# Performance work log

Measured on AMD Instinct MI355X. Metric: run time of the kernel, lower is better.

## Reference

```python
import jax, jax.numpy as jnp
import numpy as np

DECAY = 0.99
EPS = 1e-05


def setup_inputs() -> dict:
    key = jax.random.key(0)
    k1, k2, k3 = jax.random.split(key, 3)
    inp = jax.random.normal(k1, (8, 1024, 512), dtype=jnp.float32)
    embed = jax.random.normal(k2, (512, 8192), dtype=jnp.float32)
    # buffers: cluster_size starts at zeros, embed_avg is a clone of embed in torch
    cluster_size = jnp.zeros((8192,), dtype=jnp.float32)
    embed_avg = embed
    return {"input": inp, "embed": embed, "cluster_size": cluster_size, "embed_avg": embed_avg}


def reference(input, embed, cluster_size, embed_avg):
    dim, n_embed = embed.shape
    flatten = input.reshape(-1, dim)  # [N, dim]
    # squared euclidean distance via expansion: ||f||^2 - 2 f.E + ||E||^2 -> [N, n_embed]
    dist = ((flatten ** 2).sum(axis=1, keepdims=True)
            - 2.0 * flatten @ embed
            + (embed ** 2).sum(axis=0, keepdims=True))
    embed_ind_flat = jnp.argmin(dist, axis=1)  # argmax of -dist == argmin of dist
    embed_ind = embed_ind_flat.reshape(input.shape[:-1])
    # nearest-codebook lookup: F.embedding(ind, embed.T)
    quantize = jnp.take(embed.T, embed_ind, axis=0)  # [..., dim]
    # training-mode EMA statistics (one-hot scatter sums, done without a dense one-hot)
    onehot_sum = jnp.zeros((n_embed,), flatten.dtype).at[embed_ind_flat].add(1.0)
    embed_sum = jax.ops.segment_sum(flatten, embed_ind_flat, num_segments=n_embed).T  # [dim, n_embed]
    new_cluster_size = cluster_size * DECAY + (1.0 - DECAY) * onehot_sum
    new_embed_avg = embed_avg * DECAY + (1.0 - DECAY) * embed_sum
    n = new_cluster_size.sum()
    cs = (new_cluster_size + EPS) / (n + n_embed * EPS) * n
    new_embed = new_embed_avg / cs[None, :]
    # commitment loss (quantize detached) and straight-through estimator
    diff = jnp.mean((jax.lax.stop_gradient(quantize) - input) ** 2)
    quantize_st = input + jax.lax.stop_gradient(quantize - input)
    return (quantize_st, diff, embed_ind, new_embed, new_cluster_size, new_embed_avg)
```

## Files before the change

### kernel.cpp

```cpp
#include <hip/hip_runtime.h>


constexpr int N = 8192;
constexpr int K = 512;
constexpr int M = 8192;

typedef unsigned short ushortT;
typedef __attribute__((ext_vector_type(8))) short s8v;
typedef __attribute__((ext_vector_type(4))) float f4v;

__device__ __forceinline__ ushortT f2bf(float x) {
    unsigned u = __float_as_uint(x);
    unsigned r = (u + 0x7FFFu + ((u >> 16) & 1u)) >> 16;
    return (ushortT)r;
}
__device__ __forceinline__ float bf2f(ushortT h) {
    return __uint_as_float(((unsigned)h) << 16);
}

typedef const __attribute__((address_space(1))) unsigned gau;
typedef __attribute__((address_space(3))) unsigned lau;
__device__ __forceinline__ void gl16(const void* g, void* l) {
    __builtin_amdgcn_global_load_lds((gau*)g, (lau*)l, 16, 0, 0);
}

__device__ __forceinline__ unsigned packDI(float d, int col) {
    unsigned u = __float_as_uint(d);
    unsigned s = (u & 0x80000000u) ? ~u : (u | 0x80000000u);
    return (s & ~0x1FFFu) | (unsigned)col;
}
__device__ __forceinline__ float unpackD(unsigned p) {
    unsigned s = p & ~0x1FFFu;
    unsigned u = (s & 0x80000000u) ? (s & 0x7fffffffu) : ~s;
    return __uint_as_float(u);
}
__device__ __forceinline__ void top2u(unsigned& a, unsigned& b, unsigned c) {
    unsigned mn = c < a ? c : a;
    unsigned mx = c < a ? a : c;
    a = mn;
    b = mx < b ? mx : b;
}

__global__ __launch_bounds__(256) void k_prep(
    const float* __restrict__ f, const float* __restrict__ E,
    ushortT* __restrict__ Fh, ushortT* __restrict__ EhT, ushortT* __restrict__ ElT,
    float* __restrict__ pc, float* __restrict__ counts) {
    __shared__ float tile[64][65];
    int b = blockIdx.x, t = threadIdx.x;
    if (b < 2048) {
        if (b < 32) counts[b * 256 + t] = 0.f;
        size_t i8 = ((size_t)b * 256 + t) * 8;
        float4 x0 = *(const float4*)&f[i8];
        float4 x1 = *(const float4*)&f[i8 + 4];
        float xs[8] = {x0.x, x0.y, x0.z, x0.w, x1.x, x1.y, x1.z, x1.w};
        union { s8v v; ushortT u[8]; } h;
#pragma unroll
        for (int j = 0; j < 8; ++j) h.u[j] = f2bf(xs[j]);
        *(s8v*)&Fh[i8] = h.v;
    } else {
        int bb = b - 2048;
        int jb = bb & 127, kb = bb >> 7;
        int jj = t & 63, kk0 = t >> 6;
        int j0 = jb * 64, k0 = kb * 64;
#pragma unroll
        for (int it = 0; it < 16; ++it) {
            int kk = it * 4 + kk0;
            tile[kk][jj] = E[(size_t)(k0 + kk) * M + j0 + jj];
        }
        __syncthreads();
        int r = t >> 2, ks = (t & 3) * 16;
        union { s8v v[2]; ushortT u[16]; } h, lo;
        float nrm = 0.f;
#pragma unroll
        for (int i = 0; i < 16; ++i) {
            float x = tile[ks + i][r];
            nrm = fmaf(x, x, nrm);
            ushortT hh = f2bf(x);
            h.u[i] = hh;
            lo.u[i] = f2bf(x - bf2f(hh));
        }
        size_t o = (size_t)(j0 + r) * K + k0 + ks;
        *(s8v*)&EhT[o] = h.v[0];
        *(s8v*)&EhT[o + 8] = h.v[1];
        *(s8v*)&ElT[o] = lo.v[0];
        *(s8v*)&ElT[o + 8] = lo.v[1];
        nrm += __shfl_down(nrm, 2);
        nrm += __shfl_down(nrm, 1);
        if ((t & 3) == 0) pc[(size_t)kb * M + j0 + r] = nrm;
    }
}

__global__ __launch_bounds__(512) void k_score(
    const ushortT* __restrict__ Fh, const ushortT* __restrict__ Eh,
    const float* __restrict__ pc, unsigned* __restrict__ pv) {
    __shared__ alignas(16) ushortT ls[2][2][256 * 64];

    int bid = blockIdx.x;
    int xcd = bid & 7, local = bid >> 3;
    int rb = xcd * 4 + (local & 3);
    int cb = local >> 2;
    int rowBase = rb * 256, colBase = cb * 256;
    int tid = threadIdx.x;
    int w = tid >> 6, l = tid & 63;
    int wr = w >> 2, wc = w & 3;
    int l15 = l & 15, g4 = l >> 4;
    int s7 = l15 & 7;

    const ushortT* srcA = Fh + (size_t)(rowBase + w * 32) * K;
    const ushortT* srcB = Eh + (size_t)(colBase + w * 32) * K;

    f4v acc[8][4];
#pragma unroll
    for (int m = 0; m < 8; ++m)
#pragma unroll
        for (int n = 0; n < 4; ++n) acc[m][n] = (f4v){0.f, 0.f, 0.f, 0.f};

#define STAGE(p, ch)                                                  \
    do {                                                              \
        _Pragma("unroll")                                             \
        for (int i_ = 0; i_ < 4; ++i_) {                              \
            int q_ = i_ * 64 + l;                                     \
            int row_ = q_ >> 3, slot_ = q_ & 7;                       \
            int swz_ = (slot_ ^ (row_ & 7)) * 8;                      \
            size_t so_ = (size_t)row_ * K + (ch) * 64 + swz_;         \
            gl16(srcA + so_, &ls[p][0][w * 2048 + q_ * 8]);           \
            gl16(srcB + so_, &ls[p][1][w * 2048 + q_ * 8]);           \
        }                                                             \
    } while (0)

    STAGE(0, 0);
    __syncthreads();

#pragma unroll
    for (int ch = 0; ch < 8; ++ch) {
        int p = ch & 1;
        if (ch < 7) STAGE(p ^ 1, ch + 1);
#pragma unroll
        for (int kk = 0; kk < 2; ++kk) {
            s8v a[8], b[4];
#pragma unroll
            for (int m = 0; m < 8; ++m) {
                int rA = wr * 128 + m * 16 + l15;
                a[m] = *(const s8v*)&ls[p][0][rA * 64 + ((kk * 4 + g4) ^ s7) * 8];
            }
#pragma unroll
            for (int n = 0; n < 4; ++n) {
                int rB = wc * 64 + n * 16 + l15;
                b[n] = *(const s8v*)&ls[p][1][rB * 64 + ((kk * 4 + g4) ^ s7) * 8];
            }
#pragma unroll
            for (int m = 0; m < 8; ++m)
#pragma unroll
                for (int n = 0; n < 4; ++n)
                    acc[m][n] = __builtin_amdgcn_mfma_f32_16x16x32_bf16(
                        a[m], b[n], acc[m][n], 0, 0, 0);
        }
        __syncthreads();
    }
#undef STAGE

    float cj[4];
#pragma unroll
    for (int n = 0; n < 4; ++n) {
        int col = colBase + wc * 64 + n * 16 + l15;
        float s = 0.f;
#pragma unroll
        for (int kb = 0; kb < 8; ++kb) s += pc[(size_t)kb * M + col];
        cj[n] = s;
    }
    unsigned* cand = (unsigned*)ls;

#pragma unroll
    for (int m = 0; m < 8; ++m)
#pragma unroll
        for (int q = 0; q < 4; ++q) {
            unsigned p0 = packDI(fmaf(-2.f, acc[m][0][q], cj[0]), colBase + wc * 64 + l15);
            unsigned p1 = packDI(fmaf(-2.f, acc[m][1][q], cj[1]), colBase + wc * 64 + 16 + l15);
            unsigned p2 = packDI(fmaf(-2.f, acc[m][2][q], cj[2]), colBase + wc * 64 + 32 + l15);
            unsigned p3 = packDI(fmaf(-2.f, acc[m][3][q], cj[3]), colBase + wc * 64 + 48 + l15);
            unsigned a_ = p0 < p1 ? p0 : p1;
            unsigned b_ = p0 < p1 ? p1 : p0;
            top2u(a_, b_, p2);
            top2u(a_, b_, p3);
#pragma unroll
            for (int mk = 8; mk >= 2; mk >>= 1) {
                unsigned oa = __shfl_xor((int)a_, mk);
                unsigned ob = __shfl_xor((int)b_, mk);
                top2u(a_, b_, oa);
                top2u(a_, b_, ob);
            }
            if (l15 < 2) {
                int row = wr * 128 + m * 16 + g4 * 4 + q;
                int slot = wc * 4 + l15 * 2;
                cand[row * 17 + slot] = a_;
                cand[row * 17 + slot + 1] = b_;
            }
        }
    __syncthreads();
    if (tid < 256) {
        unsigned best = cand[tid * 17], second = cand[tid * 17 + 1];
#pragma unroll
        for (int i = 2; i < 16; i += 2) {
            top2u(best, second, cand[tid * 17 + i]);
            top2u(best, second, cand[tid * 17 + i + 1]);
        }
        size_t o = (size_t)(rowBase + tid) * 64 + cb * 2;
        pv[o] = best;
        pv[o + 1] = second;
    }
}

__global__ __launch_bounds__(256) void k_combine(
    const unsigned* __restrict__ pv, const float* __restrict__ f,
    const ushortT* __restrict__ EhT, const ushortT* __restrict__ ElT,
    const float* __restrict__ pc,
    int* __restrict__ indws, float* __restrict__ o_ind, float* __restrict__ counts,
    float* __restrict__ o_q, float* __restrict__ diffp) {
    __shared__ float dsum[4];
    int w = threadIdx.x >> 6, l = threadIdx.x & 63;
    int row = blockIdx.x * 4 + w;
    unsigned e = pv[(size_t)row * 64 + l];
    unsigned mn = e;
#pragma unroll
    for (int m = 1; m < 64; m <<= 1) {
        unsigned o = __shfl_xor((int)mn, m);
        mn = o < mn ? o : mn;
    }
    float thr = unpackD(mn) + 2.0f;
    float dl = unpackD(e);
    float bestd = 3.4e38f; int bestj = 0x7fffffff;
    float4 fa = *(const float4*)&f[(size_t)row * K + l * 8];
    float4 fb = *(const float4*)&f[(size_t)row * K + l * 8 + 4];
    float fx[8] = {fa.x, fa.y, fa.z, fa.w, fb.x, fb.y, fb.z, fb.w};
    s8v qh, ql;
    unsigned long long mask = __ballot(dl <= thr);
    while (mask) {
        int b = __ffsll(mask) - 1;
        mask &= mask - 1;
        int j = (int)(__shfl((int)e, b) & 0x1fff);
        s8v hv = *(const s8v*)(EhT + (size_t)j * K + l * 8);
        s8v lv = *(const s8v*)(ElT + (size_t)j * K + l * 8);
        float a = 0.f;
#pragma unroll
        for (int q = 0; q < 8; ++q)
            a = fmaf(fx[q], bf2f((ushortT)hv[q]) + bf2f((ushortT)lv[q]), a);
#pragma unroll
        for (int m = 1; m < 64; m <<= 1) a += __shfl_xor(a, m);
        float cj = 0.f;
#pragma unroll
        for (int kb = 0; kb < 8; ++kb) cj += pc[(size_t)kb * M + j];
        float d = cj - 2.f * a;
        if (d < bestd || (d == bestd && j < bestj)) {
            bestd = d; bestj = j; qh = hv; ql = lv;
        }
    }
    float os[8];
    float local = 0.f;
#pragma unroll
    for (int q = 0; q < 8; ++q) {
        float qv = bf2f((ushortT)qh[q]) + bf2f((ushortT)ql[q]);
        float d = qv - fx[q];
        os[q] = fx[q] + d;
        local = fmaf(d, d, local);
    }
    float4 o0 = {os[0], os[1], os[2], os[3]};
    float4 o1 = {os[4], os[5], os[6], os[7]};
    *(float4*)&o_q[(size_t)row * K + l * 8] = o0;
    *(float4*)&o_q[(size_t)row * K + l * 8 + 4] = o1;
#pragma unroll
    for (int m = 1; m < 64; m <<= 1) local += __shfl_xor(local, m);
    if (l == 0) {
        indws[row] = bestj;
        o_ind[row] = (float)bestj;
        atomicAdd(&counts[bestj], 1.0f);
        dsum[w] = local;
    }
    __syncthreads();
    if (threadIdx.x == 0)
        diffp[blockIdx.x] = dsum[0] + dsum[1] + dsum[2] + dsum[3];
}

__global__ __launch_bounds__(256) void k_ema(
    const float* __restrict__ f, const int* __restrict__ indws,
    const float* __restrict__ ea, float* __restrict__ o_avg, float* __restrict__ o_ne,
    const float* __restrict__ cs_in, const float* __restrict__ counts,
    float* __restrict__ o_ncs,
    const float* __restrict__ diffp, float* __restrict__ o_diff) {
    int b = blockIdx.x, t = threadIdx.x;
    __shared__ float wsum[4];
    if (b == 256) {
#pragma unroll 32
        for (int i = 0; i < 32; ++i) {
            int j = i * 256 + t;
            o_ncs[j] = 0.99f * cs_in[j] + 0.01f * counts[j];
        }
        float dl = 0.f;
#pragma unroll
        for (int i = 0; i < 8; ++i) dl += diffp[i * 256 + t];
#pragma unroll
        for (int off = 32; off; off >>= 1) dl += __shfl_down(dl, off);
        if ((t & 63) == 0) wsum[t >> 6] = dl;
        __syncthreads();
        if (t == 0)
            o_diff[0] = (wsum[0] + wsum[1] + wsum[2] + wsum[3]) * (1.0f / 4194304.0f);
        return;
    }
    __shared__ float acc[512 * 33];
    __shared__ int q[8192];
    __shared__ int qn;
    __shared__ float csr_s[32];
    __shared__ float nsh;
    for (int i = t; i < 512 * 33; i += 256) acc[i] = 0.f;
    if (t == 0) qn = 0;
    __syncthreads();
    for (int r = t; r < N; r += 256) {
        int j = indws[r];
        if ((j >> 5) == b) {
            int s = atomicAdd(&qn, 1);
            q[s] = (r << 5) | (j & 31);
        }
    }
    __syncthreads();
    int nq = qn;
    int s = 0;
    for (; s + 4 <= nq; s += 4) {
        int e0 = q[s], e1 = q[s + 1], e2 = q[s + 2], e3 = q[s + 3];
        float a0 = f[(size_t)(e0 >> 5) * K + t],       c0 = f[(size_t)(e0 >> 5) * K + t + 256];
        float a1 = f[(size_t)(e1 >> 5) * K + t],       c1 = f[(size_t)(e1 >> 5) * K + t + 256];
        float a2 = f[(size_t)(e2 >> 5) * K + t],       c2 = f[(size_t)(e2 >> 5) * K + t + 256];
        float a3 = f[(size_t)(e3 >> 5) * K + t],       c3 = f[(size_t)(e3 >> 5) * K + t + 256];
        acc[t * 33 + (e0 & 31)] += a0;         acc[(t + 256) * 33 + (e0 & 31)] += c0;
        acc[t * 33 + (e1 & 31)] += a1;         acc[(t + 256) * 33 + (e1 & 31)] += c1;
        acc[t * 33 + (e2 & 31)] += a2;         acc[(t + 256) * 33 + (e2 & 31)] += c2;
        acc[t * 33 + (e3 & 31)] += a3;         acc[(t + 256) * 33 + (e3 & 31)] += c3;
    }
    for (; s < nq; ++s) {
        int e = q[s];
        float a0 = f[(size_t)(e >> 5) * K + t];
        float c0 = f[(size_t)(e >> 5) * K + t + 256];
        acc[t * 33 + (e & 31)] += a0;
        acc[(t + 256) * 33 + (e & 31)] += c0;
    }
    float loc = 0.f;
#pragma unroll 32
    for (int i = 0; i < 32; ++i) {
        int j = i * 256 + t;
        loc += 0.99f * cs_in[j] + 0.01f * counts[j];
    }
#pragma unroll
    for (int off = 32; off; off >>= 1) loc += __shfl_down(loc, off);
    __syncthreads();
    if ((t & 63) == 0) wsum[t >> 6] = loc;
    __syncthreads();
    if (t == 0) nsh = wsum[0] + wsum[1] + wsum[2] + wsum[3];
    __syncthreads();
    if (t < 32) {
        int j = b * 32 + t;
        float v = 0.99f * cs_in[j] + 0.01f * counts[j];
        float n = nsh;
        csr_s[t] = (v + 1e-5f) / (n + 8192.0f * 1e-5f) * n;
    }
    __syncthreads();
    for (int i = t; i < 512 * 32; i += 256) {
        int d = i >> 5, c = i & 31;
        size_t o = (size_t)d * M + b * 32 + c;
        float val = 0.99f * ea[o] + 0.01f * acc[d * 33 + c];
        o_avg[o] = val;
        o_ne[o] = val / csr_s[c];
    }
}

extern "C" void kernel_launch(void* const* d_in, const int* in_sizes, int n_in,
                              void* d_out, int out_size, void* d_ws, size_t ws_size,
                              hipStream_t stream) {
    const float* f     = (const float*)d_in[0];
    const float* E     = (const float*)d_in[1];
    const float* cs_in = (const float*)d_in[2];
    const float* ea    = (const float*)d_in[3];

    float* out = (float*)d_out;
    float* o_q    = out;
    float* o_diff = out + 4194304;
    float* o_ind  = out + 4194305;
    float* o_ne   = out + 4202497;
    float* o_ncs  = out + 8396801;
    float* o_avg  = out + 8404993;

    ushortT* Fh  = (ushortT*)o_q;
    ushortT* EhT = (ushortT*)o_ne;
    ushortT* ElT = EhT + (size_t)M * K;
    unsigned* pv = (unsigned*)o_avg;

    float* wsf    = (float*)d_ws;
    float* counts = wsf + 8192;
    int*   indws  = (int*)(wsf + 24576);
    float* diffp  = wsf + 32768;
    float* pc     = wsf + 40960;

    k_prep   <<<3072, 256, 0, stream>>>(f, E, Fh, EhT, ElT, pc, counts);
    k_score  <<<1024, 512, 0, stream>>>(Fh, EhT, pc, pv);
    k_combine<<<2048, 256, 0, stream>>>(pv, f, EhT, ElT, pc, indws, o_ind, counts,
                                        o_q, diffp);
    k_ema    <<<257, 256, 0, stream>>>(f, indws, ea, o_avg, o_ne,
                                       cs_in, counts, o_ncs,
                                       diffp, o_diff);
}
```

Before: 161.2 us.

## Switch candidate-scoring GEMM from bf16 to fp8 MFMA with wider rescoring margin

Inputs and codebook are quantized to fp8 in the prep kernel, and the scoring GEMM uses the fp8 16x16x32 MFMA with half-size LDS tiles and adjusted swizzling. Halving operand bytes is meant to cut global/LDS traffic and raise matrix throughput. Because fp8 scores are coarser, the combine kernel's candidate threshold is widened, so more candidates get exact rescoring. The risks are more rescoring work and the true nearest code falling outside the margin.

```diff
diff --git a/kernel.cpp b/kernel.cpp
--- a/kernel.cpp
+++ b/kernel.cpp
@@ -6,6 +6,7 @@
 constexpr int M = 8192;
 
 typedef unsigned short ushortT;
+typedef long long i64;
 typedef __attribute__((ext_vector_type(8))) short s8v;
 typedef __attribute__((ext_vector_type(4))) float f4v;
 
@@ -43,7 +44,8 @@
 
 __global__ __launch_bounds__(256) void k_prep(
     const float* __restrict__ f, const float* __restrict__ E,
-    ushortT* __restrict__ Fh, ushortT* __restrict__ EhT, ushortT* __restrict__ ElT,
+    char* __restrict__ F8, char* __restrict__ E8T,
+    ushortT* __restrict__ EhT, ushortT* __restrict__ ElT,
     float* __restrict__ pc, float* __restrict__ counts) {
     __shared__ float tile[64][65];
     int b = blockIdx.x, t = threadIdx.x;
@@ -52,11 +54,12 @@
         size_t i8 = ((size_t)b * 256 + t) * 8;
         float4 x0 = *(const float4*)&f[i8];
         float4 x1 = *(const float4*)&f[i8 + 4];
-        float xs[8] = {x0.x, x0.y, x0.z, x0.w, x1.x, x1.y, x1.z, x1.w};
-        union { s8v v; ushortT u[8]; } h;
-#pragma unroll
-        for (int j = 0; j < 8; ++j) h.u[j] = f2bf(xs[j]);
-        *(s8v*)&Fh[i8] = h.v;
+        int w0 = __builtin_amdgcn_cvt_pk_fp8_f32(x0.x, x0.y, 0, 0);
+        w0 = __builtin_amdgcn_cvt_pk_fp8_f32(x0.z, x0.w, w0, 1);
+        int w1 = __builtin_amdgcn_cvt_pk_fp8_f32(x1.x, x1.y, 0, 0);
+        w1 = __builtin_amdgcn_cvt_pk_fp8_f32(x1.z, x1.w, w1, 1);
+        int2 pk = {w0, w1};
+        *(int2*)&F8[i8] = pk;
     } else {
         int bb = b - 2048;
         int jb = bb & 127, kb = bb >> 7;
@@ -70,10 +73,12 @@
         __syncthreads();
         int r = t >> 2, ks = (t & 3) * 16;
         union { s8v v[2]; ushortT u[16]; } h, lo;
+        float xs[16];
         float nrm = 0.f;
 #pragma unroll
         for (int i = 0; i < 16; ++i) {
             float x = tile[ks + i][r];
+            xs[i] = x;
             nrm = fmaf(x, x, nrm);
             ushortT hh = f2bf(x);
             h.u[i] = hh;
@@ -84,6 +89,17 @@
         *(s8v*)&EhT[o + 8] = h.v[1];
         *(s8v*)&ElT[o] = lo.v[0];
         *(s8v*)&ElT[o + 8] = lo.v[1];
+        int4 pk;
+        int w_;
+        w_ = __builtin_amdgcn_cvt_pk_fp8_f32(xs[0], xs[1], 0, 0);
+        pk.x = __builtin_amdgcn_cvt_pk_fp8_f32(xs[2], xs[3], w_, 1);
+        w_ = __builtin_amdgcn_cvt_pk_fp8_f32(xs[4], xs[5], 0, 0);
+        pk.y = __builtin_amdgcn_cvt_pk_fp8_f32(xs[6], xs[7], w_, 1);
+        w_ = __builtin_amdgcn_cvt_pk_fp8_f32(xs[8], xs[9], 0, 0);
+        pk.z = __builtin_amdgcn_cvt_pk_fp8_f32(xs[10], xs[11], w_, 1);
+        w_ = __builtin_amdgcn_cvt_pk_fp8_f32(xs[12], xs[13], 0, 0);
+        pk.w = __builtin_amdgcn_cvt_pk_fp8_f32(xs[14], xs[15], w_, 1);
+        *(int4*)&E8T[o] = pk;
         nrm += __shfl_down(nrm, 2);
         nrm += __shfl_down(nrm, 1);
         if ((t & 3) == 0) pc[(size_t)kb * M + j0 + r] = nrm;
@@ -91,9 +107,9 @@
 }
 
 __global__ __launch_bounds__(512) void k_score(
-    const ushortT* __restrict__ Fh, const ushortT* __restrict__ Eh,
+    const char* __restrict__ F8, const char* __restrict__ E8,
     const float* __restrict__ pc, unsigned* __restrict__ pv) {
-    __shared__ alignas(16) ushortT ls[2][2][256 * 64];
+    __shared__ alignas(16) char ls[2][2][256 * 64];
 
     int bid = blockIdx.x;
     int xcd = bid & 7, local = bid >> 3;
@@ -104,10 +120,9 @@
     int w = tid >> 6, l = tid & 63;
     int wr = w >> 2, wc = w & 3;
     int l15 = l & 15, g4 = l >> 4;
-    int s7 = l15 & 7;
-
-    const ushortT* srcA = Fh + (size_t)(rowBase + w * 32) * K;
-    const ushortT* srcB = Eh + (size_t)(colBase + w * 32) * K;
+
+    const char* srcA = F8 + (size_t)(rowBase + w * 32) * 512;
+    const char* srcB = E8 + (size_t)(colBase + w * 32) * 512;
 
     f4v acc[8][4];
 #pragma unroll
@@ -118,13 +133,13 @@
 #define STAGE(p, ch)                                                  \
     do {                                                              \
         _Pragma("unroll")                                             \
-        for (int i_ = 0; i_ < 4; ++i_) {                              \
+        for (int i_ = 0; i_ < 2; ++i_) {                              \
             int q_ = i_ * 64 + l;                                     \
-            int row_ = q_ >> 3, slot_ = q_ & 7;                       \
-            int swz_ = (slot_ ^ (row_ & 7)) * 8;                      \
-            size_t so_ = (size_t)row_ * K + (ch) * 64 + swz_;         \
-            gl16(srcA + so_, &ls[p][0][w * 2048 + q_ * 8]);           \
-            gl16(srcB + so_, &ls[p][1][w * 2048 + q_ * 8]);           \
+            int row_ = q_ >> 2, slot_ = q_ & 3;                       \
+            int swz_ = (slot_ ^ (row_ & 3)) * 16;                     \
+            size_t so_ = (size_t)row_ * 512 + (ch) * 64 + swz_;       \
+            gl16(srcA + so_, &ls[p][0][w * 2048 + q_ * 16]);          \
+            gl16(srcB + so_, &ls[p][1][w * 2048 + q_ * 16]);          \
         }                                                             \
     } while (0)
 
@@ -137,22 +152,26 @@
         if (ch < 7) STAGE(p ^ 1, ch + 1);
 #pragma unroll
         for (int kk = 0; kk < 2; ++kk) {
-            s8v a[8], b[4];
+            i64 a[8], b[4];
 #pragma unroll
             for (int m = 0; m < 8; ++m) {
                 int rA = wr * 128 + m * 16 + l15;
-                a[m] = *(const s8v*)&ls[p][0][rA * 64 + ((kk * 4 + g4) ^ s7) * 8];
+                int off = rA * 64 + (((kk * 2 + (g4 >> 1)) ^ (rA & 3)) * 16)
+                          + (g4 & 1) * 8;
+                a[m] = *(const i64*)&ls[p][0][off];
             }
 #pragma unroll
             for (int n = 0; n < 4; ++n) {
                 int rB = wc * 64 + n * 16 + l15;
-                b[n] = *(const s8v*)&ls[p][1][rB * 64 + ((kk * 4 + g4) ^ s7) * 8];
+                int off = rB * 64 + (((kk * 2 + (g4 >> 1)) ^ (rB & 3)) * 16)
+                          + (g4 & 1) * 8;
+                b[n] = *(const i64*)&ls[p][1][off];
             }
 #pragma unroll
             for (int m = 0; m < 8; ++m)
 #pragma unroll
                 for (int n = 0; n < 4; ++n)
-                    acc[m][n] = __builtin_amdgcn_mfma_f32_16x16x32_bf16(
+                    acc[m][n] = __builtin_amdgcn_mfma_f32_16x16x32_fp8_fp8(
                         a[m], b[n], acc[m][n], 0, 0, 0);
         }
         __syncthreads();
@@ -226,7 +245,7 @@
         unsigned o = __shfl_xor((int)mn, m);
         mn = o < mn ? o : mn;
     }
-    float thr = unpackD(mn) + 2.0f;
+    float thr = unpackD(mn) + 17.0f;
     float dl = unpackD(e);
     float bestd = 3.4e38f; int bestj = 0x7fffffff;
     float4 fa = *(const float4*)&f[(size_t)row * K + l * 8];
@@ -386,7 +405,8 @@
     float* o_ncs  = out + 8396801;
     float* o_avg  = out + 8404993;
 
-    ushortT* Fh  = (ushortT*)o_q;
+    char* F8  = (char*)o_q;
+    char* E8T = F8 + (size_t)N * K;
     ushortT* EhT = (ushortT*)o_ne;
     ushortT* ElT = EhT + (size_t)M * K;
     unsigned* pv = (unsigned*)o_avg;
@@ -397,8 +417,8 @@
     float* diffp  = wsf + 32768;
     float* pc     = wsf + 40960;
 
-    k_prep   <<<3072, 256, 0, stream>>>(f, E, Fh, EhT, ElT, pc, counts);
-    k_score  <<<1024, 512, 0, stream>>>(Fh, EhT, pc, pv);
+    k_prep   <<<3072, 256, 0, stream>>>(f, E, F8, E8T, EhT, ElT, pc, counts);
+    k_score  <<<1024, 512, 0, stream>>>(F8, E8T, pc, pv);
     k_combine<<<2048, 256, 0, stream>>>(pv, f, EhT, ElT, pc, indws, o_ind, counts,
                                         o_q, diffp);
     k_ema    <<<257, 256, 0, stream>>>(f, indws, ea, o_avg, o_ne,
```

New measurement: 176.3 us. 9.3% more time.
